# Kernel tuning notes

Hardware: AMD Instinct MI355X
Metric: run time of the kernel (lower is better)

The kernel has to match this reference:

```python
import jax, jax.numpy as jnp
import numpy as np

HEADS = 4
EPS_LN = 1e-6
EPS_IN = 1e-5


def _ln(x, g, b):
    m = x.mean(-1, keepdims=True)
    v = ((x - m) ** 2).mean(-1, keepdims=True)
    return (x - m) / jnp.sqrt(v + EPS_LN) * g + b


def _inorm(s):
    # nn.InstanceNorm2d(1) (affine=False): normalize each (batch, channel=head)
    # slice over the last two (N, N) dims, biased variance, eps=1e-5.
    m = s.mean((-2, -1), keepdims=True)
    v = ((s - m) ** 2).mean((-2, -1), keepdims=True)
    return (s - m) / jnp.sqrt(v + EPS_IN)


def setup_inputs() -> dict:
    key = jax.random.key(0)
    ks = jax.random.split(key, 32)
    B, C, Hh = 8, 256, HEADS
    sc = 1.0 / np.sqrt(C)

    def n(k, shape, s):
        return jax.random.normal(k, shape, jnp.float32) * s

    return {
        "x": n(ks[0], (B, C, 6, 6, 6), 1.0),
        # global branch params
        "g_tok_w": n(ks[1], (C,), 0.05), "g_tok_b": jnp.zeros((C,), jnp.float32),
        "g_ln1_g": jnp.ones((C,), jnp.float32), "g_ln1_b": jnp.zeros((C,), jnp.float32),
        "g_wq": n(ks[2], (C, C * Hh), sc), "g_wk": n(ks[3], (C, C * Hh), sc),
        "g_wv": n(ks[4], (C, C * Hh), sc), "g_wo": n(ks[5], (C * Hh, C), sc),
        "g_ln2_g": jnp.ones((C,), jnp.float32), "g_ln2_b": jnp.zeros((C,), jnp.float32),
        "g_mo_w": n(ks[6], (C, C), sc), "g_mo_b": jnp.zeros((C,), jnp.float32),
        # local branch params
        "l_pw": n(ks[7], (8, 8), 0.35), "l_pb": jnp.zeros((8,), jnp.float32),
        "l_ln1_g": jnp.ones((C,), jnp.float32), "l_ln1_b": jnp.zeros((C,), jnp.float32),
        "l_wq": n(ks[8], (C, C * Hh), sc), "l_wk": n(ks[9], (C, C * Hh), sc),
        "l_wv": n(ks[10], (C, C * Hh), sc), "l_wo": n(ks[11], (C * Hh, C), sc),
        "l_ln2_g": jnp.ones((C,), jnp.float32), "l_ln2_b": jnp.zeros((C,), jnp.float32),
        "l_mo_w": n(ks[12], (C, C), sc), "l_mo_b": jnp.zeros((C,), jnp.float32),
    }


def _global_branch(x, tok_w, tok_b, ln1_g, ln1_b, wq, wk, wv, wo, ln2_g, ln2_b, mo_w, mo_b):
    B, C, D, H, W = x.shape
    Hh = HEADS
    # TokenLearner_Global: conv1x1x1 (1->256) then mean over (D,H,W), then
    # view(B,C,C).mean(dim=1).  Since the conv is 1x1 on a single input channel,
    # this collapses exactly to: w * mean(x over C,D,H,W) + b.
    m = x.mean((1, 2, 3, 4))                       # (B,)
    tok = m[:, None] * tok_w + tok_b               # (B, C)
    res = tok
    t = _ln(tok, ln1_g, ln1_b)                     # (B, C)
    q = (t @ wq).reshape(B, Hh, C)                 # heads outer in the 1024 split
    k = (t @ wk).reshape(B, Hh, C)
    v = (t @ wv).reshape(B, Hh, C)
    # mh_q^T (B,h,C,1) @ mh_k (B,h,1,C) -> rank-1 (B,h,C,C) score map
    score = q[:, :, :, None] * k[:, :, None, :]
    a = jax.nn.softmax(_inorm(score), axis=-1)
    o = jnp.einsum('bhij,bhj->bhi', a, v)          # attn @ mh_v^T -> (B,h,C)
    # permute(0,3,2,1).view: flatten as (c, heads) with c outer
    o = o.transpose(0, 2, 1).reshape(B, C * Hh)
    out = o @ wo                                   # (B, C)
    tok2 = _ln(out + res, ln2_g, ln2_b)            # (B, C)
    # map_out conv1x1 + GELU on a spatially-constant expand -> compute once
    g = jax.nn.gelu(jnp.einsum('bc,oc->bo', tok2, mo_w) + mo_b, approximate=False)
    return jnp.broadcast_to(g[:, :, None, None, None], (B, C, D, H, W))


def _local_branch(x, pw, pb, ln1_g, ln1_b, wq, wk, wv, wo, ln2_g, ln2_b, mo_w, mo_b):
    B, C, D, H, W = x.shape
    Hh = HEADS
    # TokenLearner_Local: conv3d(1->8, k=2, s=2) per channel == patchify 2x2x2
    xp = x.reshape(B * C, 3, 2, 3, 2, 3, 2).transpose(0, 1, 3, 5, 2, 4, 6)
    xp = xp.reshape(B * C, 27, 8)                  # (BC, patches, patch_vol)
    tok = xp @ pw.T + pb                           # (BC, 27, 8) embed_dim=8
    tok = tok.reshape(B, C, 3, 3, 3, 2, 2, 2)
    # res: (b c)(d h w)(p1 p2 p3) -> b (d p1 h p2 w p3) c
    res = tok.transpose(0, 2, 5, 3, 6, 4, 7, 1).reshape(B, 216, C)
    # attn input: (b c)(d h w)(p1 p2 p3) -> (b d h w) (p1 p2 p3) c
    e = tok.reshape(B, C, 3, 3, 3, 8).transpose(0, 2, 3, 4, 5, 1).reshape(B * 27, 8, C)
    e = _ln(e, ln1_g, ln1_b)
    # (c heads) split: c outer, heads inner
    q = (e @ wq).reshape(B * 27, 8, C, Hh).transpose(0, 3, 2, 1)   # (B27,h,C,8)
    k = (e @ wk).reshape(B * 27, 8, C, Hh).transpose(0, 3, 1, 2)   # (B27,h,8,C)
    v = (e @ wv).reshape(B * 27, 8, C, Hh).transpose(0, 3, 2, 1)   # (B27,h,C,8)
    score = q @ k                                                  # (B27,h,C,C)
    a = jax.nn.softmax(_inorm(score), axis=-1)
    o = a @ v                                                      # (B27,h,C,8)
    # (b d h w) heads c (p1 p2 p3) -> b (d p1 h p2 w p3) (c heads)
    o = o.reshape(B, 3, 3, 3, Hh, C, 2, 2, 2)
    o = o.transpose(0, 1, 6, 2, 7, 3, 8, 5, 4).reshape(B, 216, C * Hh)
    out = o @ wo                                                   # (B,216,C)
    t2 = _ln(out + res, ln2_g, ln2_b)
    xm = t2.transpose(0, 2, 1).reshape(B, C, D, H, W)
    return jax.nn.gelu(
        jnp.einsum('bcdhw,oc->bodhw', xm, mo_w) + mo_b[None, :, None, None, None],
        approximate=False)


def reference(x,
              g_tok_w, g_tok_b, g_ln1_g, g_ln1_b, g_wq, g_wk, g_wv, g_wo,
              g_ln2_g, g_ln2_b, g_mo_w, g_mo_b,
              l_pw, l_pb, l_ln1_g, l_ln1_b, l_wq, l_wk, l_wv, l_wo,
              l_ln2_g, l_ln2_b, l_mo_w, l_mo_b):
    g = _global_branch(x, g_tok_w, g_tok_b, g_ln1_g, g_ln1_b, g_wq, g_wk, g_wv,
                       g_wo, g_ln2_g, g_ln2_b, g_mo_w, g_mo_b)
    l = _local_branch(x, l_pw, l_pb, l_ln1_g, l_ln1_b, l_wq, l_wk, l_wv,
                      l_wo, l_ln2_g, l_ln2_b, l_mo_w, l_mo_b)
    return x + g + l
```

## Files before the change

### kernel.cpp

```cpp
#include <hip/hip_runtime.h>
#include <stdint.h>
#include <math.h>

#define DEVFN __device__ __forceinline__
typedef unsigned short u16;
typedef short bf16x8 __attribute__((ext_vector_type(8)));
typedef float f32x4  __attribute__((ext_vector_type(4)));

DEVFN float blk_sum(float v, float* s4) {
  #pragma unroll
  for (int o = 32; o > 0; o >>= 1) v += __shfl_down(v, o, 64);
  __syncthreads();
  if ((threadIdx.x & 63) == 0) s4[threadIdx.x >> 6] = v;
  __syncthreads();
  return s4[0] + s4[1] + s4[2] + s4[3];
}

DEVFN void blk_sum2(float a, float b, float* out, float (*s)[4]) {
  #pragma unroll
  for (int o = 32; o > 0; o >>= 1) {
    a += __shfl_down(a, o, 64);
    b += __shfl_down(b, o, 64);
  }
  __syncthreads();
  if ((threadIdx.x & 63) == 0) {
    int wi = threadIdx.x >> 6;
    s[0][wi] = a; s[1][wi] = b;
  }
  __syncthreads();
  out[0] = s[0][0] + s[0][1] + s[0][2] + s[0][3];
  out[1] = s[1][0] + s[1][1] + s[1][2] + s[1][3];
}

DEVFN void blk_sum17(float* v, float (*s)[4]) {
  #pragma unroll
  for (int o = 32; o > 0; o >>= 1)
    #pragma unroll
    for (int i = 0; i < 17; ++i) v[i] += __shfl_down(v[i], o, 64);
  __syncthreads();
  if ((threadIdx.x & 63) == 0) {
    int wi = threadIdx.x >> 6;
    #pragma unroll
    for (int i = 0; i < 17; ++i) s[i][wi] = v[i];
  }
  __syncthreads();
  #pragma unroll
  for (int i = 0; i < 17; ++i) v[i] = s[i][0] + s[i][1] + s[i][2] + s[i][3];
}

DEVFN float gelu_f(float x) {
  return 0.5f * x * (1.f + erff(x * 0.7071067811865475f));
}

DEVFN u16 bf16_rne(float f) {
  uint32_t u = __float_as_uint(f);
  return (u16)((u + 0x7fffu + ((u >> 16) & 1u)) >> 16);
}

DEVFN float bf2f(u16 v) { return __uint_as_float(((uint32_t)v) << 16); }

DEVFN void gload16(const u16* g, u16* l) {
  auto gp = (const __attribute__((address_space(1))) uint32_t*)(uintptr_t)g;
  auto lp = (__attribute__((address_space(3))) uint32_t*)(uintptr_t)l;
  __builtin_amdgcn_global_load_lds(gp, lp, 16, 0, 0);
}

DEVFN void stageCM(const u16* G, size_t gstride, u16* L, int w, int lane) {
  #pragma unroll
  for (int i = 0; i < 8; ++i) {
    int c16 = w * 8 + i;
    gload16(G + (size_t)lane * gstride + c16 * 8, L + c16 * 512);
  }
}

DEVFN void stageCM32(const u16* G, size_t gstride, u16* L, int w, int lane) {
  int row = lane & 31, ch = lane >> 5;
  #pragma unroll
  for (int i = 0; i < 4; ++i) {
    int c16 = w * 8 + i * 2 + ch;
    gload16(G + (size_t)row * gstride + c16 * 8, L + (w * 8 + i * 2) * 256);
  }
}

DEVFN void trc_tile(const float* __restrict__ in, u16* __restrict__ out,
                    int R, int C, int r0, int c0, float (*tile)[33], int tid) {
  int tx = tid & 31, ty = tid >> 5;
  for (int i = ty; i < 32; i += 8) tile[i][tx] = in[(size_t)(r0 + i) * C + c0 + tx];
  __syncthreads();
  for (int i = ty; i < 32; i += 8)
    out[(size_t)(c0 + i) * R + r0 + tx] = bf16_rne(tile[tx][i]);
}

__global__ __launch_bounds__(256) void k_l_tok_prep(
    const float* __restrict__ x, const float* __restrict__ pw,
    const float* __restrict__ pb, const float* __restrict__ g1,
    const float* __restrict__ b1, float* __restrict__ res,
    u16* __restrict__ eln_bf, float* __restrict__ g_part,
    const float* __restrict__ wq, const float* __restrict__ wk,
    const float* __restrict__ wv, const float* __restrict__ wo,
    const float* __restrict__ mow, u16* __restrict__ WcatT,
    u16* __restrict__ woT, u16* __restrict__ moB) {
  __shared__ __align__(16) char smem[8448];
  int bid0 = blockIdx.x, tid = threadIdx.x;
  if (bid0 < 216) {
    float* pws = (float*)smem;
    float (*s17)[4] = (float(*)[4])(smem + 256);
    int b = bid0 / 27, patch = bid0 % 27;
    int pz = patch / 9, py = (patch / 3) % 3, px = patch % 3;
    int c = tid;
    if (c < 64) pws[c] = pw[c];
    __syncthreads();
    const float* xb = x + (size_t)(b * 256 + c) * 216 + (2 * pz) * 36 + (2 * py) * 6 + 2 * px;
    float2 t00 = *(const float2*)&xb[0],  t01 = *(const float2*)&xb[6];
    float2 t10 = *(const float2*)&xb[36], t11 = *(const float2*)&xb[42];
    float xv[8] = {t00.x, t00.y, t01.x, t01.y, t10.x, t10.y, t11.x, t11.y};
    float v[8];
    #pragma unroll
    for (int p = 0; p < 8; ++p) {
      float a = pb[p];
      #pragma unroll
      for (int j = 0; j < 8; ++j) a = fmaf(xv[j], pws[p * 8 + j], a);
      v[p] = a;
    }
    float sums[17];
    sums[0] = xv[0] + xv[1] + xv[2] + xv[3] + xv[4] + xv[5] + xv[6] + xv[7];
    #pragma unroll
    for (int p = 0; p < 8; ++p) { sums[1 + p] = v[p]; sums[9 + p] = v[p] * v[p]; }
    blk_sum17(sums, s17);
    if (c == 0) g_part[bid0] = sums[0];
    float gg = g1[c], bb = b1[c];
    #pragma unroll
    for (int p = 0; p < 8; ++p) {
      int sz = 2 * pz + (p >> 2), sy = 2 * py + ((p >> 1) & 1), sx = 2 * px + (p & 1);
      int t = b * 216 + sz * 36 + sy * 6 + sx;
      float mu = sums[1 + p] * (1.f / 256.f);
      float var = sums[9 + p] * (1.f / 256.f) - mu * mu;
      res[t * 256 + c] = v[p];
      eln_bf[t * 256 + c] = bf16_rne((v[p] - mu) * rsqrtf(var + 1e-6f) * gg + bb);
    }
  } else {
    float (*tile)[33] = (float(*)[33])smem;
    int bid = bid0 - 216;
    if (bid < 768) {
      int which = bid >> 8, b2 = bid & 255;
      const float* in = (which == 0) ? wq : (which == 1) ? wk : wv;
      u16* out = WcatT + which * 262144;
      int r0 = (b2 & 7) * 32, c0 = (b2 >> 3) * 32;
      trc_tile(in, out, 256, 1024, r0, c0, tile, tid);
    } else if (bid < 1024) {
      int b2 = bid - 768;
      int r0 = (b2 & 31) * 32, c0 = (b2 >> 5) * 32;
      trc_tile(wo, woT, 1024, 256, r0, c0, tile, tid);
    } else {
      int i = (bid - 1024) * 256 + tid;
      moB[i] = bf16_rne(mow[i]);
    }
  }
}

__global__ __launch_bounds__(256) void k_gemm_qkv_fused(
    const u16* __restrict__ A, const u16* __restrict__ BT, u16* __restrict__ C,
    const float* __restrict__ g_part, const float* __restrict__ tw_,
    const float* __restrict__ tb_, const float* __restrict__ g1,
    const float* __restrict__ b1, const float* __restrict__ wq,
    const float* __restrict__ wk, const float* __restrict__ wv,
    float* __restrict__ gqkv) {
  __shared__ __align__(16) char smem[65536];
  int bid = blockIdx.x, tid = threadIdx.x;
  if (bid < 48) {
    float* ts = (float*)smem;
    float (*red)[4][8] = (float(*)[4][8])(smem + 8192);
    float* s4 = (float*)(smem + 16384);
    float* m_s = (float*)(smem + 16400);
    float tw = tw_[tid], tb = tb_[tid], gg = g1[tid], bb = b1[tid];
    float S1 = blk_sum(tw, s4);
    float S2 = blk_sum(tw * tw, s4);
    float S3 = blk_sum(tb, s4);
    float S4 = blk_sum(tb * tb, s4);
    float S5 = blk_sum(tw * tb, s4);
    {
      int b = tid >> 5, sl = tid & 31;
      float a = (sl < 27) ? g_part[b * 27 + sl] : 0.f;
      #pragma unroll
      for (int o = 16; o > 0; o >>= 1) a += __shfl_down(a, o, 32);
      if (sl == 0) m_s[b] = a * (1.f / 55296.f);
    }
    __syncthreads();
    #pragma unroll
    for (int b = 0; b < 8; ++b) {
      float m = m_s[b];
      float mu = (m * S1 + S3) * (1.f / 256.f);
      float var = (m * m * S2 + 2.f * m * S5 + S4) * (1.f / 256.f) - mu * mu;
      ts[b * 256 + tid] = (m * tw + tb - mu) * rsqrtf(var + 1e-6f) * gg + bb;
    }
    __syncthreads();
    int col0 = bid * 64;
    int cl = tid & 63, kq = tid >> 6;
    int col = col0 + cl;
    int m = col >> 10, cc = col & 1023;
    const float* W = (m == 0) ? wq : (m == 1) ? wk : wv;
    float acc[8] = {};
    for (int c0 = kq * 64; c0 < kq * 64 + 64; c0 += 8) {
      float wbuf[8];
      #pragma unroll
      for (int j = 0; j < 8; ++j) wbuf[j] = W[(c0 + j) * 1024 + cc];
      #pragma unroll
      for (int j = 0; j < 8; ++j) {
        float w = wbuf[j];
        #pragma unroll
        for (int b = 0; b < 8; ++b) acc[b] = fmaf(ts[b * 256 + c0 + j], w, acc[b]);
      }
    }
    #pragma unroll
    for (int b = 0; b < 8; ++b) red[cl][kq][b] = acc[b];
    __syncthreads();
    if (kq == 0) {
      #pragma unroll
      for (int b = 0; b < 8; ++b)
        gqkv[b * 3072 + col] = red[cl][0][b] + red[cl][1][b] + red[cl][2][b] + red[cl][3][b];
    }
  } else {
    const int N = 3072, K = 256;
    u16* aL = (u16*)smem;
    u16* bL = (u16*)smem + 16384;
    int t0 = bid - 48;
    int tile = (t0 & 7) * 162 + (t0 >> 3);
    int rowblk = (tile % 27) * 64, colblk = (tile / 27) * 64;
    int lane = tid & 63, w = tid >> 6;
    int wr = (w >> 1) * 32, wc = (w & 1) * 32;
    int fm = lane & 15, lg = lane >> 4;
    stageCM(A + (size_t)rowblk * K, K, aL, w, lane);
    stageCM(BT + (size_t)colblk * K, K, bL, w, lane);
    __syncthreads();
    f32x4 acc[2][2] = {};
    #pragma unroll
    for (int kk = 0; kk < 8; ++kk) {
      int k16 = kk * 4 + lg;
      bf16x8 bn0 = *(const bf16x8*)&bL[k16 * 512 + (wc + fm) * 8];
      bf16x8 bn1 = *(const bf16x8*)&bL[k16 * 512 + (wc + 16 + fm) * 8];
      bf16x8 af0 = *(const bf16x8*)&aL[k16 * 512 + (wr + fm) * 8];
      bf16x8 af1 = *(const bf16x8*)&aL[k16 * 512 + (wr + 16 + fm) * 8];
      acc[0][0] = __builtin_amdgcn_mfma_f32_16x16x32_bf16(af0, bn0, acc[0][0], 0, 0, 0);
      acc[0][1] = __builtin_amdgcn_mfma_f32_16x16x32_bf16(af0, bn1, acc[0][1], 0, 0, 0);
      acc[1][0] = __builtin_amdgcn_mfma_f32_16x16x32_bf16(af1, bn0, acc[1][0], 0, 0, 0);
      acc[1][1] = __builtin_amdgcn_mfma_f32_16x16x32_bf16(af1, bn1, acc[1][1], 0, 0, 0);
    }
    __syncthreads();
    u16* ct = aL;
    #pragma unroll
    for (int mi = 0; mi < 2; ++mi)
      #pragma unroll
      for (int ni = 0; ni < 2; ++ni)
        #pragma unroll
        for (int r = 0; r < 4; ++r)
          ct[(wr + mi * 16 + lg * 4 + r) * 72 + wc + ni * 16 + fm] = bf16_rne(acc[mi][ni][r]);
    __syncthreads();
    #pragma unroll
    for (int pass = 0; pass < 2; ++pass) {
      int id = pass * 256 + tid;
      int r = id >> 3, u = id & 7;
      *(uint4*)&C[(size_t)(rowblk + r) * N + colblk + u * 8] = *(uint4*)&ct[r * 72 + u * 8];
    }
  }
}

__global__ __launch_bounds__(256) void k_l_attn_fused(
    const u16* __restrict__ qkv, u16* __restrict__ o_buf,
    const float* __restrict__ gq, float* __restrict__ g_o) {
  __shared__ __align__(16) uint4 Qb[256], Kb[256];
  __shared__ __align__(16) u16 vt[16][264];
  __shared__ __align__(16) u16 Pl[256][72];
  __shared__ float rqA[64][4], rkA[64][4], rlq[64][4], rlk[64][4], s_ab[2];
  int bid = blockIdx.x, tid = threadIdx.x;
  if (bid < 32) {
    float* ks = (float*)Qb;
    float* vs = ks + 256;
    float* s4 = (float*)Kb;
    int b = bid >> 2, h = bid & 3;
    int i = tid;
    const float* base = gq + b * 3072 + h * 256;
    float q = base[i];
    float k = base[1024 + i];
    ks[i] = k;
    vs[i] = base[2048 + i];
    float sq  = blk_sum(q, s4);
    float sq2 = blk_sum(q * q, s4);
    float sk  = blk_sum(k, s4);
    float sk2 = blk_sum(k * k, s4);
    float tot  = sq * sk * (1.f / 65536.f);
    float tot2 = sq2 * sk2 * (1.f / 65536.f);
    float rstd = rsqrtf(tot2 - tot * tot + 1e-5f);
    float A = rstd, B = -tot * rstd;
    float den = 0.f, num = 0.f;
    for (int j = 0; j < 256; ++j) {
      float w = __expf(fmaf(q * ks[j], A, B));
      den += w; num += w * vs[j];
    }
    g_o[b * 1024 + (i << 2) + h] = num / den;
    return;
  }
  int nb = bid - 32;
  int n = nb >> 2, h = nb & 3;
  int b = n / 27, patch = n % 27;
  int bz = 2 * (patch / 9), by = 2 * ((patch / 3) % 3), bx = 2 * (patch % 3);
  {
    int c = tid;
    u16 qv[8], kv[8], vv[8];
    #pragma unroll
    for (int p = 0; p < 8; ++p) {
      int t_l = b * 216 + (bz + (p >> 2)) * 36 + (by + ((p >> 1) & 1)) * 6 + (bx + (p & 1));
      const u16* row = qkv + (size_t)t_l * 3072 + (c << 2) + h;
      qv[p] = row[0]; kv[p] = row[1024]; vv[p] = row[2048];
    }
    uint32_t qw[4], kw[4];
    #pragma unroll
    for (int i = 0; i < 4; ++i) {
      qw[i] = (uint32_t)qv[2 * i] | ((uint32_t)qv[2 * i + 1] << 16);
      kw[i] = (uint32_t)kv[2 * i] | ((uint32_t)kv[2 * i + 1] << 16);
    }
    Qb[c] = make_uint4(qw[0], qw[1], qw[2], qw[3]);
    Kb[c] = make_uint4(kw[0], kw[1], kw[2], kw[3]);
    #pragma unroll
    for (int p = 0; p < 8; ++p) vt[p][c] = vv[p];
    vt[8][c] = 0x3F80u;
    #pragma unroll
    for (int r2 = 9; r2 < 16; ++r2) vt[r2][c] = 0;
  }
  __syncthreads();
  {
    int p = tid & 63, chunk = tid >> 6;
    int d = p >> 3, e = p & 7;
    float aq = 0.f, ak = 0.f, lq = 0.f, lk = 0.f;
    for (int cc = chunk * 64; cc < chunk * 64 + 64; ++cc) {
      const u16* qr = (const u16*)&Qb[cc];
      const u16* kr = (const u16*)&Kb[cc];
      float qd = bf2f(qr[d]), qe = bf2f(qr[e]);
      float kd = bf2f(kr[d]), ke = bf2f(kr[e]);
      aq = fmaf(qd, qe, aq); ak = fmaf(kd, ke, ak);
      if (e == 0) { lq += qd; lk += kd; }
    }
    rqA[p][chunk] = aq; rkA[p][chunk] = ak; rlq[p][chunk] = lq; rlk[p][chunk] = lk;
    __syncthreads();
    if (tid < 64) {
      float gq2 = rqA[tid][0] + rqA[tid][1] + rqA[tid][2] + rqA[tid][3];
      float gk = rkA[tid][0] + rkA[tid][1] + rkA[tid][2] + rkA[tid][3];
      float vprod = gq2 * gk, vmu = 0.f;
      if ((tid & 7) == 0) {
        float slq = rlq[tid][0] + rlq[tid][1] + rlq[tid][2] + rlq[tid][3];
        float slk = rlk[tid][0] + rlk[tid][1] + rlk[tid][2] + rlk[tid][3];
        vmu = slq * slk;
      }
      #pragma unroll
      for (int o = 32; o > 0; o >>= 1) {
        vprod += __shfl_down(vprod, o, 64);
        vmu   += __shfl_down(vmu, o, 64);
      }
      if (tid == 0) {
        float mu = vmu * (1.f / 65536.f), m2 = vprod * (1.f / 65536.f);
        float rstd = rsqrtf(m2 - mu * mu + 1e-5f);
        s_ab[0] = rstd; s_ab[1] = -mu * rstd;
      }
    }
    __syncthreads();
  }
  float Af = s_ab[0], Bf = s_ab[1];
  int lane = tid & 63, w = tid >> 6;
  int l15 = lane & 15, lg = lane >> 4;
  bf16x8 qf[4];
  #pragma unroll
  for (int qt = 0; qt < 4; ++qt)
    qf[qt] = *(const bf16x8*)&Qb[w * 64 + qt * 16 + l15];
  f32x4 acc_o[4] = {};
  #pragma unroll 1
  for (int jc = 0; jc < 4; ++jc) {
    bf16x8 kf[4];
    #pragma unroll
    for (int jt = 0; jt < 4; ++jt) {
      bf16x8 z = {};
      if (lg == 0) z = *(const bf16x8*)&Kb[jc * 64 + jt * 16 + l15];
      kf[jt] = z;
    }
    #pragma unroll
    for (int jt = 0; jt < 4; ++jt) {
      #pragma unroll
      for (int qt = 0; qt < 4; ++qt) {
        f32x4 zc = {};
        f32x4 s = __builtin_amdgcn_mfma_f32_16x16x32_bf16(kf[jt], qf[qt], zc, 0, 0, 0);
        float e0 = __expf(fmaf(s[0], Af, Bf));
        float e1 = __expf(fmaf(s[1], Af, Bf));
        float e2 = __expf(fmaf(s[2], Af, Bf));
        float e3 = __expf(fmaf(s[3], Af, Bf));
        uint32_t w0 = (__float_as_uint(e0) >> 16) | (__float_as_uint(e1) & 0xFFFF0000u);
        uint32_t w1 = (__float_as_uint(e2) >> 16) | (__float_as_uint(e3) & 0xFFFF0000u);
        int q = w * 64 + qt * 16 + l15;
        *(uint2*)&Pl[q][jt * 16 + lg * 4] = make_uint2(w0, w1);
      }
    }
    #pragma unroll
    for (int ks2 = 0; ks2 < 2; ++ks2) {
      bf16x8 vf = *(const bf16x8*)&vt[l15][jc * 64 + ks2 * 32 + lg * 8];
      #pragma unroll
      for (int qt = 0; qt < 4; ++qt) {
        bf16x8 pf = *(const bf16x8*)&Pl[w * 64 + qt * 16 + l15][ks2 * 32 + lg * 8];
        acc_o[qt] = __builtin_amdgcn_mfma_f32_16x16x32_bf16(pf, vf, acc_o[qt], 0, 0, 0);
      }
    }
  }
  int src = ((lane & 48) + 8) << 2;
  int p = l15;
  int t_l = b * 216 + (bz + (p >> 2)) * 36 + (by + ((p >> 1) & 1)) * 6 + (bx + (p & 1));
  #pragma unroll
  for (int qt = 0; qt < 4; ++qt) {
    #pragma unroll
    for (int r = 0; r < 4; ++r) {
      float den = __int_as_float(__builtin_amdgcn_ds_bpermute(src, __float_as_int(acc_o[qt][r])));
      if (p < 8) {
        int q = w * 64 + qt * 16 + lg * 4 + r;
        o_buf[(size_t)t_l * 1024 + (q << 2) + h] = bf16_rne(acc_o[qt][r] / den);
      }
    }
  }
}

__global__ __launch_bounds__(256) void k_gemm_sk_fused(
    const u16* __restrict__ A, const u16* __restrict__ BT, float* __restrict__ Cp,
    const float* __restrict__ g_o, const float* __restrict__ wo,
    float* __restrict__ part) {
  __shared__ __align__(16) char smem[65536];
  int bid = blockIdx.x, tid = threadIdx.x;
  if (bid < 32) {
    float* os = (float*)smem;
    int kc = bid;
    os[tid] = g_o[(tid >> 5) * 1024 + kc * 32 + (tid & 31)];
    __syncthreads();
    float acc[8] = {};
    #pragma unroll
    for (int kk = 0; kk < 32; ++kk) {
      float w = wo[(size_t)(kc * 32 + kk) * 256 + tid];
      #pragma unroll
      for (int b = 0; b < 8; ++b) acc[b] = fmaf(os[b * 32 + kk], w, acc[b]);
    }
    #pragma unroll
    for (int b = 0; b < 8; ++b) part[kc * 2048 + b * 256 + tid] = acc[b];
  } else {
    const int M = 1728, N = 256, K = 1024;
    u16* aL = (u16*)smem;
    u16* bL = (u16*)smem + 16384;
    int bid2 = bid - 32;
    int rowblk = (bid2 % 27) * 64, colblk = ((bid2 / 27) & 3) * 64;
    int kz = bid2 / 108;
    float* C = Cp + (size_t)kz * M * N;
    int lane = tid & 63, w = tid >> 6;
    int wr = (w >> 1) * 32, wc = (w & 1) * 32;
    int fm = lane & 15, lg = lane >> 4;
    f32x4 acc[2][2] = {};
    #pragma unroll 1
    for (int step = 0; step < 2; ++step) {
      int kt = kz * 512 + step * 256;
      __syncthreads();
      stageCM(A + (size_t)rowblk * K + kt, K, aL, w, lane);
      stageCM(BT + (size_t)colblk * K + kt, K, bL, w, lane);
      __syncthreads();
      #pragma unroll
      for (int kk = 0; kk < 8; ++kk) {
        int k16 = kk * 4 + lg;
        bf16x8 bn0 = *(const bf16x8*)&bL[k16 * 512 + (wc + fm) * 8];
        bf16x8 bn1 = *(const bf16x8*)&bL[k16 * 512 + (wc + 16 + fm) * 8];
        bf16x8 af0 = *(const bf16x8*)&aL[k16 * 512 + (wr + fm) * 8];
        bf16x8 af1 = *(const bf16x8*)&aL[k16 * 512 + (wr + 16 + fm) * 8];
        acc[0][0] = __builtin_amdgcn_mfma_f32_16x16x32_bf16(af0, bn0, acc[0][0], 0, 0, 0);
        acc[0][1] = __builtin_amdgcn_mfma_f32_16x16x32_bf16(af0, bn1, acc[0][1], 0, 0, 0);
        acc[1][0] = __builtin_amdgcn_mfma_f32_16x16x32_bf16(af1, bn0, acc[1][0], 0, 0, 0);
        acc[1][1] = __builtin_amdgcn_mfma_f32_16x16x32_bf16(af1, bn1, acc[1][1], 0, 0, 0);
      }
    }
    __syncthreads();
    float* ct = (float*)smem;
    #pragma unroll
    for (int mi = 0; mi < 2; ++mi)
      #pragma unroll
      for (int ni = 0; ni < 2; ++ni)
        #pragma unroll
        for (int r = 0; r < 4; ++r)
          ct[(wr + mi * 16 + lg * 4 + r) * 64 + wc + ni * 16 + fm] = acc[mi][ni][r];
    __syncthreads();
    #pragma unroll
    for (int pass = 0; pass < 4; ++pass) {
      int id = pass * 256 + tid;
      int r = id >> 4, u = id & 15;
      *(float4*)&C[(size_t)(rowblk + r) * N + colblk + u * 4] = *(float4*)&ct[r * 64 + u * 4];
    }
  }
}

__global__ __launch_bounds__(256) void k_l_ln2_fused(
    const float* __restrict__ proj0, const float* __restrict__ proj1,
    const float* __restrict__ res, const float* __restrict__ g2,
    const float* __restrict__ b2, u16* __restrict__ t2b,
    const float* __restrict__ part, const float* __restrict__ g_part,
    const float* __restrict__ tw_, const float* __restrict__ tb_,
    const float* __restrict__ gg2, const float* __restrict__ gb2,
    const float* __restrict__ mow, const float* __restrict__ mob,
    float* __restrict__ g_vec) {
  __shared__ float s2v[2][4];
  __shared__ float ts[256];
  int bid = blockIdx.x, c = threadIdx.x;
  if (bid < 8) {
    int b = bid;
    float a = (c < 27) ? g_part[b * 27 + c] : 0.f;
    float m = blk_sum(a, (float*)s2v) * (1.f / 55296.f);
    float v = m * tw_[c] + tb_[c];
    #pragma unroll
    for (int kc = 0; kc < 32; ++kc) v += part[kc * 2048 + b * 256 + c];
    float r2[2];
    blk_sum2(v, v * v, r2, s2v);
    float mu = r2[0] * (1.f / 256.f);
    float var = r2[1] * (1.f / 256.f) - mu * mu;
    ts[c] = (v - mu) * rsqrtf(var + 1e-6f) * gg2[c] + gb2[c];
    __syncthreads();
    float a2 = mob[c];
    const float* wrow = mow + (size_t)c * 256;
    for (int c0 = 0; c0 < 256; c0 += 8) {
      float wbuf[8];
      #pragma unroll
      for (int j = 0; j < 8; ++j) wbuf[j] = wrow[c0 + j];
      #pragma unroll
      for (int j = 0; j < 8; ++j) a2 = fmaf(ts[c0 + j], wbuf[j], a2);
    }
    g_vec[b * 256 + c] = gelu_f(a2);
  } else {
    int t = bid - 8;
    float v = proj0[t * 256 + c] + proj1[t * 256 + c] + res[t * 256 + c];
    float r2[2];
    blk_sum2(v, v * v, r2, s2v);
    float mu = r2[0] * (1.f / 256.f);
    float var = r2[1] * (1.f / 256.f) - mu * mu;
    t2b[t * 256 + c] = bf16_rne((v - mu) * rsqrtf(var + 1e-6f) * g2[c] + b2[c]);
  }
}

__global__ __launch_bounds__(256) void k_gemm_mo_final(
    const u16* __restrict__ A, const u16* __restrict__ BT,
    const float* __restrict__ x, const float* __restrict__ gvec,
    const float* __restrict__ mob, float* __restrict__ out) {
  __shared__ __align__(16) char smem[49152];
  u16* aL = (u16*)smem;
  u16* bL = (u16*)smem + 8192;
  float (*ct)[65] = (float(*)[65])smem;
  const int K = 256;
  int tid = threadIdx.x;
  int rowblk = blockIdx.x * 32, colblk = blockIdx.y * 64;
  int lane = tid & 63, w = tid >> 6;
  int wr = (w >> 1) * 16, wc = (w & 1) * 32;
  int fm = lane & 15, lg = lane >> 4;
  stageCM32(A + (size_t)rowblk * K, K, aL, w, lane);
  stageCM(BT + (size_t)colblk * K, K, bL, w, lane);
  __syncthreads();
  f32x4 acc[2] = {};
  #pragma unroll
  for (int kk = 0; kk < 8; ++kk) {
    int k16 = kk * 4 + lg;
    bf16x8 bn0 = *(const bf16x8*)&bL[k16 * 512 + (wc + fm) * 8];
    bf16x8 bn1 = *(const bf16x8*)&bL[k16 * 512 + (wc + 16 + fm) * 8];
    bf16x8 af0 = *(const bf16x8*)&aL[k16 * 256 + (wr + fm) * 8];
    acc[0] = __builtin_amdgcn_mfma_f32_16x16x32_bf16(af0, bn0, acc[0], 0, 0, 0);
    acc[1] = __builtin_amdgcn_mfma_f32_16x16x32_bf16(af0, bn1, acc[1], 0, 0, 0);
  }
  __syncthreads();
  int row_l0 = wr + lg * 4;
  #pragma unroll
  for (int ni = 0; ni < 2; ++ni)
    #pragma unroll
    for (int r = 0; r < 4; ++r)
      ct[row_l0 + r][wc + ni * 16 + fm] = acc[ni][r];
  __syncthreads();
  int s_l = tid & 31, half = (tid >> 5) & 1;
  #pragma unroll 4
  for (int pass = 0; pass < 8; ++pass) {
    int col_l = (tid >> 6) * 16 + pass * 2 + half;
    int row = rowblk + s_l, col = colblk + col_l;
    int b = row / 216, s = row - b * 216;
    size_t idx = (size_t)b * 55296 + (size_t)col * 216 + s;
    out[idx] = x[idx] + gvec[b * 256 + col] + gelu_f(ct[s_l][col_l] + mob[col]);
  }
}

extern "C" void kernel_launch(void* const* d_in, const int* in_sizes, int n_in,
                              void* d_out, int out_size, void* d_ws, size_t ws_size,
                              hipStream_t stream) {
  const float* x     = (const float*)d_in[0];
  const float* g_tw  = (const float*)d_in[1];
  const float* g_tb  = (const float*)d_in[2];
  const float* g_l1g = (const float*)d_in[3];
  const float* g_l1b = (const float*)d_in[4];
  const float* g_wq  = (const float*)d_in[5];
  const float* g_wk  = (const float*)d_in[6];
  const float* g_wv  = (const float*)d_in[7];
  const float* g_wo  = (const float*)d_in[8];
  const float* g_l2g = (const float*)d_in[9];
  const float* g_l2b = (const float*)d_in[10];
  const float* g_mow = (const float*)d_in[11];
  const float* g_mob = (const float*)d_in[12];
  const float* l_pw  = (const float*)d_in[13];
  const float* l_pb  = (const float*)d_in[14];
  const float* l_l1g = (const float*)d_in[15];
  const float* l_l1b = (const float*)d_in[16];
  const float* l_wq  = (const float*)d_in[17];
  const float* l_wk  = (const float*)d_in[18];
  const float* l_wv  = (const float*)d_in[19];
  const float* l_wo  = (const float*)d_in[20];
  const float* l_l2g = (const float*)d_in[21];
  const float* l_l2b = (const float*)d_in[22];
  const float* l_mow = (const float*)d_in[23];
  const float* l_mob = (const float*)d_in[24];
  float* out = (float*)d_out;
  float* ws  = (float*)d_ws;

  float* g_qkv  = ws + 4096;
  float* g_o    = ws + 28672;
  float* g_vec  = ws + 36864;
  float* g_part = ws + 38912;
  float* res    = ws + 40960;
  u16*   eln_bf = (u16*)(ws + 483328);
  u16*   WcatT  = (u16*)(ws + 704512);
  u16*   woT    = (u16*)(ws + 1097728);
  u16*   moB    = (u16*)(ws + 1228800);
  u16*   qkvb   = (u16*)(ws + 1261568);
  u16*   o_buf  = (u16*)(ws + 6569984);
  float* proj   = ws + 7454720;
  u16*   t2b    = (u16*)(ws + 8339456);
  float* part_wo= ws + 8560640;

  k_l_tok_prep<<<1496, 256, 0, stream>>>(x, l_pw, l_pb, l_l1g, l_l1b,
                                         res, eln_bf, g_part,
                                         l_wq, l_wk, l_wv, l_wo, l_mow,
                                         WcatT, woT, moB);
  k_gemm_qkv_fused<<<1344, 256, 0, stream>>>(eln_bf, WcatT, qkvb,
                                             g_part, g_tw, g_tb, g_l1g, g_l1b,
                                             g_wq, g_wk, g_wv, g_qkv);
  k_l_attn_fused<<<896, 256, 0, stream>>>(qkvb, o_buf, g_qkv, g_o);
  k_gemm_sk_fused<<<248, 256, 0, stream>>>(o_buf, woT, proj, g_o, g_wo, part_wo);
  k_l_ln2_fused<<<1736, 256, 0, stream>>>(proj, proj + 442368, res,
                                          l_l2g, l_l2b, t2b,
                                          part_wo, g_part, g_tw, g_tb,
                                          g_l2g, g_l2b, g_mow, g_mob, g_vec);
  k_gemm_mo_final<<<dim3(54, 4), 256, 0, stream>>>(t2b, moB, x, g_vec, l_mob, out);
}
```

Before: 92.52 us.

## Fuse all six stages into a persistent cooperative megakernel with grid syncs

Each stage body is pulled into a device function and a single cooperative kernel runs all six stages in turn. Blocks loop over each stage's work items, and a grid-wide barrier separates the stages. The goal is to remove the five kernel launch gaps and the tail drain between dependent kernels. In exchange every stage now runs with one shared 64KB LDS allocation and the register budget of the heaviest stage, which caps the number of resident blocks. The grid syncs also add their own cost, and the original multi-kernel path is kept as a fallback if the cooperative launch fails.

```diff
diff --git a/kernel.cpp b/kernel.cpp
--- a/kernel.cpp
+++ b/kernel.cpp
@@ -1,6 +1,9 @@
 #include <hip/hip_runtime.h>
+#include <hip/hip_cooperative_groups.h>
 #include <stdint.h>
 #include <math.h>
+
+namespace cg = cooperative_groups;
 
 #define DEVFN __device__ __forceinline__
 typedef unsigned short u16;
@@ -91,21 +94,17 @@
     out[(size_t)(c0 + i) * R + r0 + tx] = bf16_rne(tile[tx][i]);
 }
 
-__global__ __launch_bounds__(256) void k_l_tok_prep(
-    const float* __restrict__ x, const float* __restrict__ pw,
-    const float* __restrict__ pb, const float* __restrict__ g1,
-    const float* __restrict__ b1, float* __restrict__ res,
-    u16* __restrict__ eln_bf, float* __restrict__ g_part,
-    const float* __restrict__ wq, const float* __restrict__ wk,
-    const float* __restrict__ wv, const float* __restrict__ wo,
-    const float* __restrict__ mow, u16* __restrict__ WcatT,
-    u16* __restrict__ woT, u16* __restrict__ moB) {
-  __shared__ __align__(16) char smem[8448];
-  int bid0 = blockIdx.x, tid = threadIdx.x;
-  if (bid0 < 216) {
+DEVFN void p1_body(int item, int tid, char* smem,
+                   const float* x, const float* pw, const float* pb,
+                   const float* g1, const float* b1, float* res,
+                   u16* eln_bf, float* g_part,
+                   const float* wq, const float* wk, const float* wv,
+                   const float* wo, const float* mow,
+                   u16* WcatT, u16* woT, u16* moB) {
+  if (item < 216) {
     float* pws = (float*)smem;
     float (*s17)[4] = (float(*)[4])(smem + 256);
-    int b = bid0 / 27, patch = bid0 % 27;
+    int b = item / 27, patch = item % 27;
     int pz = patch / 9, py = (patch / 3) % 3, px = patch % 3;
     int c = tid;
     if (c < 64) pws[c] = pw[c];
@@ -127,7 +126,7 @@
     #pragma unroll
     for (int p = 0; p < 8; ++p) { sums[1 + p] = v[p]; sums[9 + p] = v[p] * v[p]; }
     blk_sum17(sums, s17);
-    if (c == 0) g_part[bid0] = sums[0];
+    if (c == 0) g_part[item] = sums[0];
     float gg = g1[c], bb = b1[c];
     #pragma unroll
     for (int p = 0; p < 8; ++p) {
@@ -140,7 +139,7 @@
     }
   } else {
     float (*tile)[33] = (float(*)[33])smem;
-    int bid = bid0 - 216;
+    int bid = item - 216;
     if (bid < 768) {
       int which = bid >> 8, b2 = bid & 255;
       const float* in = (which == 0) ? wq : (which == 1) ? wk : wv;
@@ -158,16 +157,13 @@
   }
 }
 
-__global__ __launch_bounds__(256) void k_gemm_qkv_fused(
-    const u16* __restrict__ A, const u16* __restrict__ BT, u16* __restrict__ C,
-    const float* __restrict__ g_part, const float* __restrict__ tw_,
-    const float* __restrict__ tb_, const float* __restrict__ g1,
-    const float* __restrict__ b1, const float* __restrict__ wq,
-    const float* __restrict__ wk, const float* __restrict__ wv,
-    float* __restrict__ gqkv) {
-  __shared__ __align__(16) char smem[65536];
-  int bid = blockIdx.x, tid = threadIdx.x;
-  if (bid < 48) {
+DEVFN void p2_body(int item, int tid, char* smem,
+                   const u16* A, const u16* BT, u16* C,
+                   const float* g_part, const float* tw_, const float* tb_,
+                   const float* g1, const float* b1,
+                   const float* wq, const float* wk, const float* wv,
+                   float* gqkv) {
+  if (item < 48) {
     float* ts = (float*)smem;
     float (*red)[4][8] = (float(*)[4][8])(smem + 8192);
     float* s4 = (float*)(smem + 16384);
@@ -194,7 +190,7 @@
       ts[b * 256 + tid] = (m * tw + tb - mu) * rsqrtf(var + 1e-6f) * gg + bb;
     }
     __syncthreads();
-    int col0 = bid * 64;
+    int col0 = item * 64;
     int cl = tid & 63, kq = tid >> 6;
     int col = col0 + cl;
     int m = col >> 10, cc = col & 1023;
@@ -223,9 +219,9 @@
     const int N = 3072, K = 256;
     u16* aL = (u16*)smem;
     u16* bL = (u16*)smem + 16384;
-    int t0 = bid - 48;
-    int tile = (t0 & 7) * 162 + (t0 >> 3);
-    int rowblk = (tile % 27) * 64, colblk = (tile / 27) * 64;
+    int t0 = item - 48;
+    int tl = (t0 & 7) * 162 + (t0 >> 3);
+    int rowblk = (tl % 27) * 64, colblk = (tl / 27) * 64;
     int lane = tid & 63, w = tid >> 6;
     int wr = (w >> 1) * 32, wc = (w & 1) * 32;
     int fm = lane & 15, lg = lane >> 4;
@@ -264,19 +260,23 @@
   }
 }
 
-__global__ __launch_bounds__(256) void k_l_attn_fused(
-    const u16* __restrict__ qkv, u16* __restrict__ o_buf,
-    const float* __restrict__ gq, float* __restrict__ g_o) {
-  __shared__ __align__(16) uint4 Qb[256], Kb[256];
-  __shared__ __align__(16) u16 vt[16][264];
-  __shared__ __align__(16) u16 Pl[256][72];
-  __shared__ float rqA[64][4], rkA[64][4], rlq[64][4], rlk[64][4], s_ab[2];
-  int bid = blockIdx.x, tid = threadIdx.x;
-  if (bid < 32) {
+DEVFN void p3_body(int item, int tid, char* smem,
+                   const u16* qkv, u16* o_buf,
+                   const float* gq, float* g_o) {
+  uint4* Qb = (uint4*)smem;
+  uint4* Kb = (uint4*)(smem + 4096);
+  u16 (*vt)[264] = (u16(*)[264])(smem + 8192);
+  u16 (*Pl)[72]  = (u16(*)[72])(smem + 16640);
+  float (*rqA)[4] = (float(*)[4])(smem + 53504);
+  float (*rkA)[4] = (float(*)[4])(smem + 54528);
+  float (*rlq)[4] = (float(*)[4])(smem + 55552);
+  float (*rlk)[4] = (float(*)[4])(smem + 56576);
+  float* s_ab = (float*)(smem + 57600);
+  if (item < 32) {
     float* ks = (float*)Qb;
     float* vs = ks + 256;
     float* s4 = (float*)Kb;
-    int b = bid >> 2, h = bid & 3;
+    int b = item >> 2, h = item & 3;
     int i = tid;
     const float* base = gq + b * 3072 + h * 256;
     float q = base[i];
@@ -299,8 +299,8 @@
     g_o[b * 1024 + (i << 2) + h] = num / den;
     return;
   }
-  int nb = bid - 32;
-  int n = nb >> 2, h = nb & 3;
+  int nb2 = item - 32;
+  int n = nb2 >> 2, h = nb2 & 3;
   int b = n / 27, patch = n % 27;
   int bz = 2 * (patch / 9), by = 2 * ((patch / 3) % 3), bx = 2 * (patch % 3);
   {
@@ -422,15 +422,12 @@
   }
 }
 
-__global__ __launch_bounds__(256) void k_gemm_sk_fused(
-    const u16* __restrict__ A, const u16* __restrict__ BT, float* __restrict__ Cp,
-    const float* __restrict__ g_o, const float* __restrict__ wo,
-    float* __restrict__ part) {
-  __shared__ __align__(16) char smem[65536];
-  int bid = blockIdx.x, tid = threadIdx.x;
-  if (bid < 32) {
+DEVFN void p4_body(int item, int tid, char* smem,
+                   const u16* A, const u16* BT, float* Cp,
+                   const float* g_o, const float* wo, float* part) {
+  if (item < 32) {
     float* os = (float*)smem;
-    int kc = bid;
+    int kc = item;
     os[tid] = g_o[(tid >> 5) * 1024 + kc * 32 + (tid & 31)];
     __syncthreads();
     float acc[8] = {};
@@ -446,7 +443,7 @@
     const int M = 1728, N = 256, K = 1024;
     u16* aL = (u16*)smem;
     u16* bL = (u16*)smem + 16384;
-    int bid2 = bid - 32;
+    int bid2 = item - 32;
     int rowblk = (bid2 % 27) * 64, colblk = ((bid2 / 27) & 3) * 64;
     int kz = bid2 / 108;
     float* C = Cp + (size_t)kz * M * N;
@@ -493,6 +490,197 @@
   }
 }
 
+DEVFN void p5_body(int item, int tid, char* smem,
+                   const float* proj0, const float* proj1, const float* res,
+                   const float* g2, const float* b2, u16* t2b,
+                   const float* part, const float* g_part,
+                   const float* tw_, const float* tb_,
+                   const float* gg2, const float* gb2,
+                   const float* mow, const float* mob, float* g_vec) {
+  float (*s2v)[4] = (float(*)[4])smem;
+  float* ts = (float*)(smem + 64);
+  int c = tid;
+  if (item < 8) {
+    int b = item;
+    float a = (c < 27) ? g_part[b * 27 + c] : 0.f;
+    float m = blk_sum(a, (float*)s2v) * (1.f / 55296.f);
+    float v = m * tw_[c] + tb_[c];
+    #pragma unroll
+    for (int kc = 0; kc < 32; ++kc) v += part[kc * 2048 + b * 256 + c];
+    float r2[2];
+    blk_sum2(v, v * v, r2, s2v);
+    float mu = r2[0] * (1.f / 256.f);
+    float var = r2[1] * (1.f / 256.f) - mu * mu;
+    ts[c] = (v - mu) * rsqrtf(var + 1e-6f) * gg2[c] + gb2[c];
+    __syncthreads();
+    float a2 = mob[c];
+    const float* wrow = mow + (size_t)c * 256;
+    for (int c0 = 0; c0 < 256; c0 += 8) {
+      float wbuf[8];
+      #pragma unroll
+      for (int j = 0; j < 8; ++j) wbuf[j] = wrow[c0 + j];
+      #pragma unroll
+      for (int j = 0; j < 8; ++j) a2 = fmaf(ts[c0 + j], wbuf[j], a2);
+    }
+    g_vec[b * 256 + c] = gelu_f(a2);
+  } else {
+    int t = item - 8;
+    float v = proj0[t * 256 + c] + proj1[t * 256 + c] + res[t * 256 + c];
+    float r2[2];
+    blk_sum2(v, v * v, r2, s2v);
+    float mu = r2[0] * (1.f / 256.f);
+    float var = r2[1] * (1.f / 256.f) - mu * mu;
+    t2b[t * 256 + c] = bf16_rne((v - mu) * rsqrtf(var + 1e-6f) * g2[c] + b2[c]);
+  }
+}
+
+DEVFN void p6_body(int item, int tid, char* smem,
+                   const u16* A, const u16* BT, const float* x,
+                   const float* gvec, const float* mob, float* out) {
+  u16* aL = (u16*)smem;
+  u16* bL = (u16*)smem + 8192;
+  float (*ct)[65] = (float(*)[65])smem;
+  const int K = 256;
+  int rowblk = (item % 54) * 32, colblk = (item / 54) * 64;
+  int lane = tid & 63, w = tid >> 6;
+  int wr = (w >> 1) * 16, wc = (w & 1) * 32;
+  int fm = lane & 15, lg = lane >> 4;
+  stageCM32(A + (size_t)rowblk * K, K, aL, w, lane);
+  stageCM(BT + (size_t)colblk * K, K, bL, w, lane);
+  __syncthreads();
+  f32x4 acc[2] = {};
+  #pragma unroll
+  for (int kk = 0; kk < 8; ++kk) {
+    int k16 = kk * 4 + lg;
+    bf16x8 bn0 = *(const bf16x8*)&bL[k16 * 512 + (wc + fm) * 8];
+    bf16x8 bn1 = *(const bf16x8*)&bL[k16 * 512 + (wc + 16 + fm) * 8];
+    bf16x8 af0 = *(const bf16x8*)&aL[k16 * 256 + (wr + fm) * 8];
+    acc[0] = __builtin_amdgcn_mfma_f32_16x16x32_bf16(af0, bn0, acc[0], 0, 0, 0);
+    acc[1] = __builtin_amdgcn_mfma_f32_16x16x32_bf16(af0, bn1, acc[1], 0, 0, 0);
+  }
+  __syncthreads();
+  int row_l0 = wr + lg * 4;
+  #pragma unroll
+  for (int ni = 0; ni < 2; ++ni)
+    #pragma unroll
+    for (int r = 0; r < 4; ++r)
+      ct[row_l0 + r][wc + ni * 16 + fm] = acc[ni][r];
+  __syncthreads();
+  int s_l = tid & 31, half = (tid >> 5) & 1;
+  #pragma unroll 4
+  for (int pass = 0; pass < 8; ++pass) {
+    int col_l = (tid >> 6) * 16 + pass * 2 + half;
+    int row = rowblk + s_l, col = colblk + col_l;
+    int b = row / 216, s = row - b * 216;
+    size_t idx = (size_t)b * 55296 + (size_t)col * 216 + s;
+    out[idx] = x[idx] + gvec[b * 256 + col] + gelu_f(ct[s_l][col_l] + mob[col]);
+  }
+}
+
+__global__ __launch_bounds__(256) void k_mega(
+    const float* x, const float* g_tw, const float* g_tb,
+    const float* g_l1g, const float* g_l1b,
+    const float* g_wq, const float* g_wk, const float* g_wv, const float* g_wo,
+    const float* g_l2g, const float* g_l2b, const float* g_mow, const float* g_mob,
+    const float* l_pw, const float* l_pb, const float* l_l1g, const float* l_l1b,
+    const float* l_wq, const float* l_wk, const float* l_wv, const float* l_wo,
+    const float* l_l2g, const float* l_l2b, const float* l_mow, const float* l_mob,
+    float* out, float* ws) {
+  __shared__ __align__(16) char smem[65536];
+  cg::grid_group grid = cg::this_grid();
+  const int nb = gridDim.x;
+  int tid = threadIdx.x;
+
+  float* g_qkv  = ws + 4096;
+  float* g_o    = ws + 28672;
+  float* g_vec  = ws + 36864;
+  float* g_part = ws + 38912;
+  float* res    = ws + 40960;
+  u16*   eln_bf = (u16*)(ws + 483328);
+  u16*   WcatT  = (u16*)(ws + 704512);
+  u16*   woT    = (u16*)(ws + 1097728);
+  u16*   moB    = (u16*)(ws + 1228800);
+  u16*   qkvb   = (u16*)(ws + 1261568);
+  u16*   o_buf  = (u16*)(ws + 6569984);
+  float* proj   = ws + 7454720;
+  u16*   t2b    = (u16*)(ws + 8339456);
+  float* part_wo= ws + 8560640;
+
+  for (int it = blockIdx.x; it < 1496; it += nb) {
+    p1_body(it, tid, smem, x, l_pw, l_pb, l_l1g, l_l1b, res, eln_bf, g_part,
+            l_wq, l_wk, l_wv, l_wo, l_mow, WcatT, woT, moB);
+    __syncthreads();
+  }
+  grid.sync();
+  for (int it = blockIdx.x; it < 1344; it += nb) {
+    p2_body(it, tid, smem, eln_bf, WcatT, qkvb, g_part, g_tw, g_tb, g_l1g, g_l1b,
+            g_wq, g_wk, g_wv, g_qkv);
+    __syncthreads();
+  }
+  grid.sync();
+  for (int it = blockIdx.x; it < 896; it += nb) {
+    p3_body(it, tid, smem, qkvb, o_buf, g_qkv, g_o);
+    __syncthreads();
+  }
+  grid.sync();
+  for (int it = blockIdx.x; it < 248; it += nb) {
+    p4_body(it, tid, smem, o_buf, woT, proj, g_o, g_wo, part_wo);
+    __syncthreads();
+  }
+  grid.sync();
+  for (int it = blockIdx.x; it < 1736; it += nb) {
+    p5_body(it, tid, smem, proj, proj + 442368, res, l_l2g, l_l2b, t2b,
+            part_wo, g_part, g_tw, g_tb, g_l2g, g_l2b, g_mow, g_mob, g_vec);
+    __syncthreads();
+  }
+  grid.sync();
+  for (int it = blockIdx.x; it < 216; it += nb) {
+    p6_body(it, tid, smem, t2b, moB, x, g_vec, l_mob, out);
+    __syncthreads();
+  }
+}
+
+__global__ __launch_bounds__(256) void k_l_tok_prep(
+    const float* __restrict__ x, const float* __restrict__ pw,
+    const float* __restrict__ pb, const float* __restrict__ g1,
+    const float* __restrict__ b1, float* __restrict__ res,
+    u16* __restrict__ eln_bf, float* __restrict__ g_part,
+    const float* __restrict__ wq, const float* __restrict__ wk,
+    const float* __restrict__ wv, const float* __restrict__ wo,
+    const float* __restrict__ mow, u16* __restrict__ WcatT,
+    u16* __restrict__ woT, u16* __restrict__ moB) {
+  __shared__ __align__(16) char smem[8448];
+  p1_body(blockIdx.x, threadIdx.x, smem, x, pw, pb, g1, b1, res, eln_bf, g_part,
+          wq, wk, wv, wo, mow, WcatT, woT, moB);
+}
+
+__global__ __launch_bounds__(256) void k_gemm_qkv_fused(
+    const u16* __restrict__ A, const u16* __restrict__ BT, u16* __restrict__ C,
+    const float* __restrict__ g_part, const float* __restrict__ tw_,
+    const float* __restrict__ tb_, const float* __restrict__ g1,
+    const float* __restrict__ b1, const float* __restrict__ wq,
+    const float* __restrict__ wk, const float* __restrict__ wv,
+    float* __restrict__ gqkv) {
+  __shared__ __align__(16) char smem[65536];
+  p2_body(blockIdx.x, threadIdx.x, smem, A, BT, C, g_part, tw_, tb_, g1, b1,
+          wq, wk, wv, gqkv);
+}
+
+__global__ __launch_bounds__(256) void k_l_attn_fused(
+    const u16* __restrict__ qkv, u16* __restrict__ o_buf,
+    const float* __restrict__ gq, float* __restrict__ g_o) {
+  __shared__ __align__(16) char smem[57664];
+  p3_body(blockIdx.x, threadIdx.x, smem, qkv, o_buf, gq, g_o);
+}
+
+__global__ __launch_bounds__(256) void k_gemm_sk_fused(
+    const u16* __restrict__ A, const u16* __restrict__ BT, float* __restrict__ Cp,
+    const float* __restrict__ g_o, const float* __restrict__ wo,
+    float* __restrict__ part) {
+  __shared__ __align__(16) char smem[65536];
+  p4_body(blockIdx.x, threadIdx.x, smem, A, BT, Cp, g_o, wo, part);
+}
+
 __global__ __launch_bounds__(256) void k_l_ln2_fused(
     const float* __restrict__ proj0, const float* __restrict__ proj1,
     const float* __restrict__ res, const float* __restrict__ g2,
@@ -502,41 +690,9 @@
     const float* __restrict__ gg2, const float* __restrict__ gb2,
     const float* __restrict__ mow, const float* __restrict__ mob,
     float* __restrict__ g_vec) {
-  __shared__ float s2v[2][4];
-  __shared__ float ts[256];
-  int bid = blockIdx.x, c = threadIdx.x;
-  if (bid < 8) {
-    int b = bid;
-    float a = (c < 27) ? g_part[b * 27 + c] : 0.f;
-    float m = blk_sum(a, (float*)s2v) * (1.f / 55296.f);
-    float v = m * tw_[c] + tb_[c];
-    #pragma unroll
-    for (int kc = 0; kc < 32; ++kc) v += part[kc * 2048 + b * 256 + c];
-    float r2[2];
-    blk_sum2(v, v * v, r2, s2v);
-    float mu = r2[0] * (1.f / 256.f);
-    float var = r2[1] * (1.f / 256.f) - mu * mu;
-    ts[c] = (v - mu) * rsqrtf(var + 1e-6f) * gg2[c] + gb2[c];
-    __syncthreads();
-    float a2 = mob[c];
-    const float* wrow = mow + (size_t)c * 256;
-    for (int c0 = 0; c0 < 256; c0 += 8) {
-      float wbuf[8];
-      #pragma unroll
-      for (int j = 0; j < 8; ++j) wbuf[j] = wrow[c0 + j];
-      #pragma unroll
-      for (int j = 0; j < 8; ++j) a2 = fmaf(ts[c0 + j], wbuf[j], a2);
-    }
-    g_vec[b * 256 + c] = gelu_f(a2);
-  } else {
-    int t = bid - 8;
-    float v = proj0[t * 256 + c] + proj1[t * 256 + c] + res[t * 256 + c];
-    float r2[2];
-    blk_sum2(v, v * v, r2, s2v);
-    float mu = r2[0] * (1.f / 256.f);
-    float var = r2[1] * (1.f / 256.f) - mu * mu;
-    t2b[t * 256 + c] = bf16_rne((v - mu) * rsqrtf(var + 1e-6f) * g2[c] + b2[c]);
-  }
+  __shared__ __align__(16) char smem[1152];
+  p5_body(blockIdx.x, threadIdx.x, smem, proj0, proj1, res, g2, b2, t2b,
+          part, g_part, tw_, tb_, gg2, gb2, mow, mob, g_vec);
 }
 
 __global__ __launch_bounds__(256) void k_gemm_mo_final(
@@ -544,45 +700,7 @@
     const float* __restrict__ x, const float* __restrict__ gvec,
     const float* __restrict__ mob, float* __restrict__ out) {
   __shared__ __align__(16) char smem[49152];
-  u16* aL = (u16*)smem;
-  u16* bL = (u16*)smem + 8192;
-  float (*ct)[65] = (float(*)[65])smem;
-  const int K = 256;
-  int tid = threadIdx.x;
-  int rowblk = blockIdx.x * 32, colblk = blockIdx.y * 64;
-  int lane = tid & 63, w = tid >> 6;
-  int wr = (w >> 1) * 16, wc = (w & 1) * 32;
-  int fm = lane & 15, lg = lane >> 4;
-  stageCM32(A + (size_t)rowblk * K, K, aL, w, lane);
-  stageCM(BT + (size_t)colblk * K, K, bL, w, lane);
-  __syncthreads();
-  f32x4 acc[2] = {};
-  #pragma unroll
-  for (int kk = 0; kk < 8; ++kk) {
-    int k16 = kk * 4 + lg;
-    bf16x8 bn0 = *(const bf16x8*)&bL[k16 * 512 + (wc + fm) * 8];
-    bf16x8 bn1 = *(const bf16x8*)&bL[k16 * 512 + (wc + 16 + fm) * 8];
-    bf16x8 af0 = *(const bf16x8*)&aL[k16 * 256 + (wr + fm) * 8];
-    acc[0] = __builtin_amdgcn_mfma_f32_16x16x32_bf16(af0, bn0, acc[0], 0, 0, 0);
-    acc[1] = __builtin_amdgcn_mfma_f32_16x16x32_bf16(af0, bn1, acc[1], 0, 0, 0);
-  }
-  __syncthreads();
-  int row_l0 = wr + lg * 4;
-  #pragma unroll
-  for (int ni = 0; ni < 2; ++ni)
-    #pragma unroll
-    for (int r = 0; r < 4; ++r)
-      ct[row_l0 + r][wc + ni * 16 + fm] = acc[ni][r];
-  __syncthreads();
-  int s_l = tid & 31, half = (tid >> 5) & 1;
-  #pragma unroll 4
-  for (int pass = 0; pass < 8; ++pass) {
-    int col_l = (tid >> 6) * 16 + pass * 2 + half;
-    int row = rowblk + s_l, col = colblk + col_l;
-    int b = row / 216, s = row - b * 216;
-    size_t idx = (size_t)b * 55296 + (size_t)col * 216 + s;
-    out[idx] = x[idx] + gvec[b * 256 + col] + gelu_f(ct[s_l][col_l] + mob[col]);
-  }
+  p6_body(blockIdx.x + blockIdx.y * 54, threadIdx.x, smem, A, BT, x, gvec, mob, out);
 }
 
 extern "C" void kernel_launch(void* const* d_in, const int* in_sizes, int n_in,
@@ -631,18 +749,38 @@
   u16*   t2b    = (u16*)(ws + 8339456);
   float* part_wo= ws + 8560640;
 
-  k_l_tok_prep<<<1496, 256, 0, stream>>>(x, l_pw, l_pb, l_l1g, l_l1b,
-                                         res, eln_bf, g_part,
-                                         l_wq, l_wk, l_wv, l_wo, l_mow,
-                                         WcatT, woT, moB);
-  k_gemm_qkv_fused<<<1344, 256, 0, stream>>>(eln_bf, WcatT, qkvb,
-                                             g_part, g_tw, g_tb, g_l1g, g_l1b,
-                                             g_wq, g_wk, g_wv, g_qkv);
-  k_l_attn_fused<<<896, 256, 0, stream>>>(qkvb, o_buf, g_qkv, g_o);
-  k_gemm_sk_fused<<<248, 256, 0, stream>>>(o_buf, woT, proj, g_o, g_wo, part_wo);
-  k_l_ln2_fused<<<1736, 256, 0, stream>>>(proj, proj + 442368, res,
-                                          l_l2g, l_l2b, t2b,
-                                          part_wo, g_part, g_tw, g_tb,
-                                          g_l2g, g_l2b, g_mow, g_mob, g_vec);
-  k_gemm_mo_final<<<dim3(54, 4), 256, 0, stream>>>(t2b, moB, x, g_vec, l_mob, out);
-}
+  bool coop_done = false;
+  int maxb = 0;
+  if (hipOccupancyMaxActiveBlocksPerMultiprocessor(&maxb, k_mega, 256, 0) == hipSuccess
+      && maxb > 0) {
+    int grid = maxb * 256;
+    if (grid > 1736) grid = 1736;
+    void* args[] = {
+      (void*)&x, (void*)&g_tw, (void*)&g_tb, (void*)&g_l1g, (void*)&g_l1b,
+      (void*)&g_wq, (void*)&g_wk, (void*)&g_wv, (void*)&g_wo,
+      (void*)&g_l2g, (void*)&g_l2b, (void*)&g_mow, (void*)&g_mob,
+      (void*)&l_pw, (void*)&l_pb, (void*)&l_l1g, (void*)&l_l1b,
+      (void*)&l_wq, (void*)&l_wk, (void*)&l_wv, (void*)&l_wo,
+      (void*)&l_l2g, (void*)&l_l2b, (void*)&l_mow, (void*)&l_mob,
+      (void*)&out, (void*)&ws};
+    if (hipLaunchCooperativeKernel((void*)k_mega, dim3(grid), dim3(256),
+                                   args, 0, stream) == hipSuccess)
+      coop_done = true;
+  }
+  if (!coop_done) {
+    k_l_tok_prep<<<1496, 256, 0, stream>>>(x, l_pw, l_pb, l_l1g, l_l1b,
+                                           res, eln_bf, g_part,
+                                           l_wq, l_wk, l_wv, l_wo, l_mow,
+                                           WcatT, woT, moB);
+    k_gemm_qkv_fused<<<1344, 256, 0, stream>>>(eln_bf, WcatT, qkvb,
+                                               g_part, g_tw, g_tb, g_l1g, g_l1b,
+                                               g_wq, g_wk, g_wv, g_qkv);
+    k_l_attn_fused<<<896, 256, 0, stream>>>(qkvb, o_buf, g_qkv, g_o);
+    k_gemm_sk_fused<<<248, 256, 0, stream>>>(o_buf, woT, proj, g_o, g_wo, part_wo);
+    k_l_ln2_fused<<<1736, 256, 0, stream>>>(proj, proj + 442368, res,
+                                            l_l2g, l_l2b, t2b,
+                                            part_wo, g_part, g_tw, g_tb,
+                                            g_l2g, g_l2b, g_mow, g_mob, g_vec);
+    k_gemm_mo_final<<<dim3(54, 4), 256, 0, stream>>>(t2b, moB, x, g_vec, l_mob, out);
+  }
+}
```

Result: slower. 278.4 us (+200.9%).
